# Performance work log

Measured on AMD Instinct MI355X. Metric: run time of the kernel, lower is better.

The kernel has to match this reference:

```python
import jax, jax.numpy as jnp
import numpy as np

# Model dims (from init_kwargs)
D_MODEL = 1024
D_STATE = 64
D_CONV = 4
EXPAND = 2
HEADDIM = 128
NGROUPS = 1
D_INNER = EXPAND * D_MODEL              # 2048
NHEADS = D_INNER // HEADDIM             # 16
CONV_DIM = D_INNER + 2 * NGROUPS * D_STATE   # 2176
D_IN_PROJ = 2 * D_INNER + 2 * NGROUPS * D_STATE + NHEADS  # 4240
BATCH, SEQLEN = 2, 2048
DT_MIN, DT_MAX, DT_FLOOR = 1e-3, 1e-1, 1e-4
RMS_EPS = 1e-5


def setup_inputs() -> dict:
    key = jax.random.key(0)
    ks = jax.random.split(key, 8)
    u = jax.random.normal(ks[0], (BATCH, SEQLEN, D_MODEL), jnp.float32)
    in_proj_w = jax.random.normal(ks[1], (D_IN_PROJ, D_MODEL), jnp.float32) * 0.02
    conv_w = jax.random.normal(ks[2], (CONV_DIM, 1, D_CONV), jnp.float32) * 0.2
    conv_b = jax.random.normal(ks[3], (CONV_DIM,), jnp.float32) * 0.02
    # dt_bias init: inverse-softplus of dt ~ LogUniform(dt_min, dt_max)
    dt = jnp.exp(jax.random.uniform(ks[4], (NHEADS,)) * (jnp.log(DT_MAX) - jnp.log(DT_MIN)) + jnp.log(DT_MIN))
    dt = jnp.maximum(dt, DT_FLOOR)
    dt_bias = dt + jnp.log(-jnp.expm1(-dt))
    A_log = jnp.log(jax.random.uniform(ks[5], (NHEADS,), minval=1.0, maxval=16.0))
    D_param = jnp.ones((NHEADS,), jnp.float32)
    norm_w = jnp.ones((D_INNER,), jnp.float32)
    out_proj_w = jax.random.normal(ks[6], (D_MODEL, D_INNER), jnp.float32) * 0.02
    return {"u": u, "in_proj_w": in_proj_w, "conv_w": conv_w, "conv_b": conv_b,
            "dt_bias": dt_bias, "A_log": A_log, "D_param": D_param,
            "norm_w": norm_w, "out_proj_w": out_proj_w}


def _mamba2_forward(u, in_proj_w, conv_w, conv_b, dt_bias, A_log, D_param, norm_w, out_proj_w):
    B, L, _ = u.shape
    zxbcdt = jnp.einsum('bld,ed->ble', u, in_proj_w)  # (B, L, D_IN_PROJ)
    z = zxbcdt[..., :D_INNER]
    xBC = zxbcdt[..., D_INNER:D_INNER + CONV_DIM]
    dt = jax.nn.softplus(zxbcdt[..., D_INNER + CONV_DIM:] + dt_bias)  # (B, L, H)

    # Depthwise causal conv1d + SiLU
    xc = jnp.swapaxes(xBC, 1, 2)  # (B, C, L)
    xc = jax.lax.conv_general_dilated(xc, conv_w, window_strides=(1,),
                                      padding=[(D_CONV - 1, 0)],
                                      feature_group_count=CONV_DIM)
    xc = jax.nn.silu(xc + conv_b[None, :, None])
    xBC = jnp.swapaxes(xc, 1, 2)  # (B, L, C)

    x = xBC[..., :D_INNER].reshape(B, L, NHEADS, HEADDIM)
    Bmat = xBC[..., D_INNER:D_INNER + D_STATE]          # (B, L, N), ngroups=1
    Cmat = xBC[..., D_INNER + D_STATE:]                 # (B, L, N)

    A = -jnp.exp(A_log)  # (H,)

    def step(state, inp):
        dt_t, x_t, B_t, C_t = inp  # (B,H), (B,H,P), (B,N), (B,N)
        dA = jnp.exp(dt_t * A)[:, :, None, None]
        state = state * dA + (dt_t[:, :, None, None] * x_t[:, :, :, None]) * B_t[:, None, None, :]
        y_t = jnp.einsum('bhpn,bn->bhp', state, C_t) + D_param[None, :, None] * x_t
        return state, y_t

    state0 = jnp.zeros((B, NHEADS, HEADDIM, D_STATE), u.dtype)
    inputs = (jnp.moveaxis(dt, 1, 0), jnp.moveaxis(x, 1, 0),
              jnp.moveaxis(Bmat, 1, 0), jnp.moveaxis(Cmat, 1, 0))
    _, ys = jax.lax.scan(step, state0, inputs)
    y = jnp.moveaxis(ys, 0, 1).reshape(B, L, D_INNER)

    # RMSNormGated (norm_before_gate=False): gate first, then normalize
    yg = y * jax.nn.silu(z)
    rms = jax.lax.rsqrt(jnp.mean(yg * yg, axis=-1, keepdims=True) + RMS_EPS)
    yn = yg * rms * norm_w

    return jnp.einsum('ble,de->bld', yn, out_proj_w)


def reference(u, in_proj_w, conv_w, conv_b, dt_bias, A_log, D_param, norm_w, out_proj_w):
    return _mamba2_forward(u, in_proj_w, conv_w, conv_b, dt_bias, A_log, D_param, norm_w, out_proj_w)
```

## Files before the change

kernel.cpp:

```cpp
#include <hip/hip_runtime.h>
#include <cstdint>
#include <cstddef>

#define D_MODEL   1024
#define D_STATE   64
#define D_CONV    4
#define HEADDIM   128
#define NHEADS    16
#define D_INNER   2048
#define CONV_DIM  2176
#define D_IN_PROJ 4240
#define NPAD      4352
#define BATCH     2
#define SEQLEN    2048
#define NROWS     (BATCH*SEQLEN)
#define CHUNK     64
#define NCHUNK    (SEQLEN/CHUNK)

using u16   = unsigned short;
using s16x8 = __attribute__((ext_vector_type(8))) short;
using f32x4 = __attribute__((ext_vector_type(4))) float;

__device__ __forceinline__ u16 f2bf(float f) {
    union { float f; unsigned u; } v; v.f = f;
    unsigned r = v.u + 0x7fffu + ((v.u >> 16) & 1u);
    return (u16)(r >> 16);
}
__device__ __forceinline__ float bf2f(u16 x) {
    union { unsigned u; float f; } v; v.u = ((unsigned)x) << 16;
    return v.f;
}

__device__ __forceinline__ void gload16(const u16* g, u16* l) {
    __builtin_amdgcn_global_load_lds(
        (const __attribute__((address_space(1))) unsigned int*)g,
        (__attribute__((address_space(3))) unsigned int*)l, 16, 0, 0);
}

__device__ __forceinline__ void cp8(const float* in, u16* out, int i) {
    const float4* p = (const float4*)(in + (size_t)i * 8);
    float4 a = p[0], b = p[1];
    u16 o[8] = {f2bf(a.x), f2bf(a.y), f2bf(a.z), f2bf(a.w),
                f2bf(b.x), f2bf(b.y), f2bf(b.z), f2bf(b.w)};
    *(uint4*)(out + (size_t)i * 8) = *(const uint4*)o;
}

#define CVT_N0 (NROWS*D_MODEL/8)
#define CVT_N1 (NPAD*128)
#define CVT_N2 (D_MODEL*D_INNER/8)
__global__ __launch_bounds__(256) void cvt_all(
    const float* __restrict__ u, const float* __restrict__ w_in,
    const float* __restrict__ w_out,
    u16* __restrict__ u_bf, u16* __restrict__ w_in_bf, u16* __restrict__ w_out_bf)
{
    int i = blockIdx.x * 256 + threadIdx.x;
    if (i < CVT_N0) {
        cp8(u, u_bf, i);
    } else if (i < CVT_N0 + CVT_N1) {
        int j = i - CVT_N0;
        int row = j >> 7, seg = j & 127;
        u16 o[8] = {0,0,0,0,0,0,0,0};
        if (row < D_IN_PROJ) {
            const float4* p = (const float4*)(w_in + (size_t)row * D_MODEL + seg * 8);
            float4 a = p[0], b = p[1];
            o[0]=f2bf(a.x); o[1]=f2bf(a.y); o[2]=f2bf(a.z); o[3]=f2bf(a.w);
            o[4]=f2bf(b.x); o[5]=f2bf(b.y); o[6]=f2bf(b.z); o[7]=f2bf(b.w);
        }
        *(uint4*)(w_in_bf + (size_t)j * 8) = *(const uint4*)o;
    } else if (i < CVT_N0 + CVT_N1 + CVT_N2) {
        cp8(w_out, w_out_bf, i - CVT_N0 - CVT_N1);
    }
}

#define CPITCH 136
__global__ __launch_bounds__(512) void gemm_in512(
    const u16* __restrict__ A, const u16* __restrict__ B, int K,
    u16* __restrict__ C0, int n1, int ld0,
    u16* __restrict__ C1, int n2, int ld1,
    u16* __restrict__ C2, int n3, int ld2)
{
    __shared__ u16 smem[4 * 128 * 64];

    const int tid  = threadIdx.x;
    const int wid  = tid >> 6;
    const int lane = tid & 63;
    const int wm   = wid >> 2, wn = wid & 3;

    const int gx   = gridDim.x;
    int orig = blockIdx.y * gx + blockIdx.x;
    const int xcd = orig & 7;
    const int loc = orig >> 3;
    const int mt  = (xcd >> 1) * 8  + (loc & 7);
    const int nt  = (xcd & 1) * 17 + (loc >> 3);
    const int m0 = mt * 128, n0 = nt * 128;

    const int lrow = lane >> 3;
    const int lseg = (lane & 7) ^ lrow;
    const u16* gA = A + (size_t)(m0 + lrow) * K + lseg * 8;
    const u16* gB = B + (size_t)(n0 + lrow) * K + lseg * 8;

    f32x4 acc[4][2];
    #pragma unroll
    for (int i = 0; i < 4; ++i)
        #pragma unroll
        for (int j = 0; j < 2; ++j)
            acc[i][j] = (f32x4){0.f, 0.f, 0.f, 0.f};

    const int fr = lane & 15, fq = lane >> 4;
    const int nstep = K >> 6;

    auto stage = [&](int buf, int k0) {
        u16* sAp = smem + buf * 8192;
        u16* sBp = smem + 16384 + buf * 8192;
        #pragma unroll
        for (int i = 0; i < 2; ++i) {
            const int r0 = (i * 8 + wid) * 8;
            gload16(gA + (size_t)r0 * K + k0, sAp + r0 * 64);
            gload16(gB + (size_t)r0 * K + k0, sBp + r0 * 64);
        }
    };

    stage(0, 0);
    int cur = 0;
    for (int step = 0; step < nstep; ++step) {
        if (step + 1 < nstep) {
            stage(cur ^ 1, (step + 1) * 64);
            asm volatile("s_waitcnt vmcnt(4)" ::: "memory");
        } else {
            asm volatile("s_waitcnt vmcnt(0)" ::: "memory");
        }
        __builtin_amdgcn_s_barrier();
        __builtin_amdgcn_sched_barrier(0);

        const u16* sAc = smem + cur * 8192;
        const u16* sBc = smem + 16384 + cur * 8192;
        #pragma unroll
        for (int ks = 0; ks < 2; ++ks) {
            s16x8 bfr[2];
            #pragma unroll
            for (int ni = 0; ni < 2; ++ni) {
                const int row = wn * 32 + ni * 16 + fr;
                const int bo = row * 128 + ((ks * 64 + fq * 16) ^ ((row & 7) << 4));
                bfr[ni] = *(const s16x8*)((const char*)sBc + bo);
            }
            #pragma unroll
            for (int mi = 0; mi < 4; ++mi) {
                const int row = wm * 64 + mi * 16 + fr;
                const int bo = row * 128 + ((ks * 64 + fq * 16) ^ ((row & 7) << 4));
                s16x8 af = *(const s16x8*)((const char*)sAc + bo);
                #pragma unroll
                for (int ni = 0; ni < 2; ++ni)
                    acc[mi][ni] = __builtin_amdgcn_mfma_f32_16x16x32_bf16(
                        af, bfr[ni], acc[mi][ni], 0, 0, 0);
            }
        }

        __builtin_amdgcn_sched_barrier(0);
        __builtin_amdgcn_s_barrier();
        cur ^= 1;
    }
    __builtin_amdgcn_sched_barrier(0);

    u16* sC = smem;
    #pragma unroll
    for (int mi = 0; mi < 4; ++mi) {
        #pragma unroll
        for (int j = 0; j < 4; ++j) {
            const int rl = wm * 64 + mi * 16 + fq * 4 + j;
            #pragma unroll
            for (int ni = 0; ni < 2; ++ni) {
                const int cl = wn * 32 + ni * 16 + fr;
                sC[rl * CPITCH + cl] = f2bf(acc[mi][ni][j]);
            }
        }
    }
    __syncthreads();
    #pragma unroll
    for (int k2 = 0; k2 < 4; ++k2) {
        const int g  = tid + k2 * 512;
        const int rl = g >> 4, cg = g & 15;
        uint4 v = *(const uint4*)&sC[rl * CPITCH + cg * 8];
        const int r = m0 + rl, c = n0 + cg * 8;
        if (c < n1)      *(uint4*)(C0 + (size_t)r * ld0 + c)        = v;
        else if (c < n2) *(uint4*)(C1 + (size_t)r * ld1 + (c - n1)) = v;
        else if (c < n3) *(uint4*)(C2 + (size_t)r * ld2 + (c - n2)) = v;
    }
}

__global__ __launch_bounds__(512) void gemm_out512(
    const u16* __restrict__ A, const u16* __restrict__ B, int K,
    float* __restrict__ C, int N)
{
    __shared__ u16 smem[4 * 128 * 64];

    const int tid  = threadIdx.x;
    const int wid  = tid >> 6;
    const int lane = tid & 63;
    const int wm   = wid >> 2, wn = wid & 3;

    const int gx   = gridDim.x;
    const int nwg  = gx * gridDim.y;
    const int cpx  = nwg >> 3;
    int orig = blockIdx.y * gx + blockIdx.x;
    int wg   = (orig & 7) * cpx + (orig >> 3);
    const int m0 = (wg / gx) * 128, n0 = (wg % gx) * 128;

    const int lrow = lane >> 3;
    const int lseg = (lane & 7) ^ lrow;
    const u16* gA = A + (size_t)(m0 + lrow) * K + lseg * 8;
    const u16* gB = B + (size_t)(n0 + lrow) * K + lseg * 8;

    f32x4 acc[4][2];
    #pragma unroll
    for (int i = 0; i < 4; ++i)
        #pragma unroll
        for (int j = 0; j < 2; ++j)
            acc[i][j] = (f32x4){0.f, 0.f, 0.f, 0.f};

    const int fr = lane & 15, fq = lane >> 4;
    const int nstep = K >> 6;

    auto stage = [&](int buf, int k0) {
        u16* sAp = smem + buf * 8192;
        u16* sBp = smem + 16384 + buf * 8192;
        #pragma unroll
        for (int i = 0; i < 2; ++i) {
            const int r0 = (i * 8 + wid) * 8;
            gload16(gA + (size_t)r0 * K + k0, sAp + r0 * 64);
            gload16(gB + (size_t)r0 * K + k0, sBp + r0 * 64);
        }
    };

    stage(0, 0);
    int cur = 0;
    for (int step = 0; step < nstep; ++step) {
        if (step + 1 < nstep) {
            stage(cur ^ 1, (step + 1) * 64);
            asm volatile("s_waitcnt vmcnt(4)" ::: "memory");
        } else {
            asm volatile("s_waitcnt vmcnt(0)" ::: "memory");
        }
        __builtin_amdgcn_s_barrier();
        __builtin_amdgcn_sched_barrier(0);

        const u16* sAc = smem + cur * 8192;
        const u16* sBc = smem + 16384 + cur * 8192;
        #pragma unroll
        for (int ks = 0; ks < 2; ++ks) {
            s16x8 bfr[2];
            #pragma unroll
            for (int ni = 0; ni < 2; ++ni) {
                const int row = wn * 32 + ni * 16 + fr;
                const int bo = row * 128 + ((ks * 64 + fq * 16) ^ ((row & 7) << 4));
                bfr[ni] = *(const s16x8*)((const char*)sBc + bo);
            }
            #pragma unroll
            for (int mi = 0; mi < 4; ++mi) {
                const int row = wm * 64 + mi * 16 + fr;
                const int bo = row * 128 + ((ks * 64 + fq * 16) ^ ((row & 7) << 4));
                s16x8 af = *(const s16x8*)((const char*)sAc + bo);
                #pragma unroll
                for (int ni = 0; ni < 2; ++ni)
                    acc[mi][ni] = __builtin_amdgcn_mfma_f32_16x16x32_bf16(
                        af, bfr[ni], acc[mi][ni], 0, 0, 0);
            }
        }

        __builtin_amdgcn_sched_barrier(0);
        __builtin_amdgcn_s_barrier();
        cur ^= 1;
    }
    __builtin_amdgcn_sched_barrier(0);

    float* sCf = (float*)smem;
    #pragma unroll
    for (int h2 = 0; h2 < 2; ++h2) {
        if (wm == h2) {
            #pragma unroll
            for (int mi = 0; mi < 4; ++mi)
                #pragma unroll
                for (int j = 0; j < 4; ++j) {
                    const int rl = mi * 16 + fq * 4 + j;
                    #pragma unroll
                    for (int ni = 0; ni < 2; ++ni) {
                        const int cl = wn * 32 + ni * 16 + fr;
                        sCf[rl * 132 + cl] = acc[mi][ni][j];
                    }
                }
        }
        __syncthreads();
        #pragma unroll
        for (int k2 = 0; k2 < 4; ++k2) {
            const int g  = tid + k2 * 512;
            const int rl = g >> 5, cg = g & 31;
            float4 v = *(const float4*)&sCf[rl * 132 + cg * 4];
            *(float4*)(C + (size_t)(m0 + h2 * 64 + rl) * N + n0 + cg * 4) = v;
        }
        __syncthreads();
    }
}

#define NCONV8 (NROWS*(CONV_DIM/8))
__global__ __launch_bounds__(256) void conv_silu_dt(
    const u16* __restrict__ xBC, const float* __restrict__ conv_w,
    const float* __restrict__ conv_b, u16* __restrict__ xconv,
    const u16* __restrict__ dtraw, const float* __restrict__ dt_bias,
    float* __restrict__ dtw)
{
    int idx = blockIdx.x * 256 + threadIdx.x;
    if (idx < NCONV8) {
        int c8  = idx % (CONV_DIM / 8);
        int row = idx / (CONV_DIM / 8);
        int l   = row % SEQLEN;
        int b   = row / SEQLEN;
        int c0  = c8 * 8;
        const u16* src = xBC + (size_t)(b * SEQLEN) * CONV_DIM + c0;

        uint4 z4 = {0u, 0u, 0u, 0u};
        uint4 v3 = *(const uint4*)(src + (size_t)l * CONV_DIM);
        uint4 v2 = (l >= 1) ? *(const uint4*)(src + (size_t)(l-1) * CONV_DIM) : z4;
        uint4 v1 = (l >= 2) ? *(const uint4*)(src + (size_t)(l-2) * CONV_DIM) : z4;
        uint4 v0 = (l >= 3) ? *(const uint4*)(src + (size_t)(l-3) * CONV_DIM) : z4;
        const u16* p0 = (const u16*)&v0; const u16* p1 = (const u16*)&v1;
        const u16* p2 = (const u16*)&v2; const u16* p3 = (const u16*)&v3;

        u16 o[8];
        #pragma unroll
        for (int j = 0; j < 8; ++j) {
            const float4 w4 = *(const float4*)(conv_w + (size_t)(c0 + j) * 4);
            float acc = conv_b[c0 + j]
                      + bf2f(p0[j]) * w4.x + bf2f(p1[j]) * w4.y
                      + bf2f(p2[j]) * w4.z + bf2f(p3[j]) * w4.w;
            o[j] = f2bf(acc / (1.f + expf(-acc)));
        }
        *(uint4*)(xconv + (size_t)row * CONV_DIM + c0) = *(const uint4*)o;
    } else {
        int k = idx - NCONV8;
        if (k < NROWS * NHEADS) {
            int h = k & (NHEADS - 1);
            float v = bf2f(dtraw[k]) + dt_bias[h];
            dtw[k] = (v > 20.f) ? v : log1pf(expf(v));
        }
    }
}

__global__ __launch_bounds__(256) void chunk_state(
    const u16* __restrict__ xconv, const float* __restrict__ dtw,
    const float* __restrict__ A_log, u16* __restrict__ Sbuf,
    float* __restrict__ Tbuf)
{
    const int blk = blockIdx.x;
    const int k  = blk & (NCHUNK-1);
    const int bh = blk >> 5;
    const int b  = bh >> 4, h = bh & 15;
    const int tid = threadIdx.x;
    const int wid = tid >> 6, lane = tid & 63;
    const float A = -expf(A_log[h]);

    __shared__ float sdt[CHUNK], sW[CHUNK], sT;
    __shared__ u16   sWB16[CHUNK * D_STATE];
    __shared__ u16   sX[CHUNK * HEADDIM];

    const int t0 = k * CHUNK;
    const u16* xc = xconv + (size_t)(b*SEQLEN + t0) * CONV_DIM;

    if (tid < CHUNK)
        sdt[tid] = dtw[(size_t)(b*SEQLEN + t0 + tid)*NHEADS + h];
    __syncthreads();
    if (tid < CHUNK) {
        float a = 0.f, pref = 0.f;
        for (int r = 0; r < CHUNK; ++r) {
            a += sdt[r] * A;
            if (r == tid) pref = a;
        }
        sW[tid] = __expf(a - pref) * sdt[tid];
        if (tid == 0) sT = a;
    }
    __syncthreads();

    #pragma unroll
    for (int c = 0; c < 4; ++c) {
        const int r = wid * 16 + c * 4 + (lane >> 4);
        const int seg = lane & 15;
        gload16(xc + (size_t)r * CONV_DIM + h * HEADDIM + seg * 8,
                sX + (wid * 16 + c * 4) * HEADDIM);
    }
    {
        const int s = tid >> 2, nb = tid & 3;
        const float wv = sW[s];
        uint4 b0 = *(const uint4*)(xc + (size_t)s*CONV_DIM + D_INNER + nb*16);
        uint4 b1 = *(const uint4*)(xc + (size_t)s*CONV_DIM + D_INNER + nb*16 + 8);
        const u16* pb0 = (const u16*)&b0; const u16* pb1 = (const u16*)&b1;
        u16 o[16];
        #pragma unroll
        for (int j = 0; j < 8; ++j) {
            o[j]     = f2bf(wv * bf2f(pb0[j]));
            o[8 + j] = f2bf(wv * bf2f(pb1[j]));
        }
        #pragma unroll
        for (int u2 = 0; u2 < 2; ++u2) {
            const int bo = s * 128 + ((nb * 32 + u2 * 16) ^ ((s & 7) << 4));
            *(uint4*)((char*)sWB16 + bo) = *(const uint4*)&o[u2 * 8];
        }
    }
    __syncthreads();

    const int nn = tid >> 4, pp = tid & 15;
    const int p0 = pp * 8, n0 = nn * 4;
    const int base16 = (nn >> 1) << 4;
    const int sub8   = (nn & 1) * 8;
    float acc[4][8];
    #pragma unroll
    for (int i = 0; i < 4; ++i)
        #pragma unroll
        for (int j = 0; j < 8; ++j) acc[i][j] = 0.f;

    for (int sb = 0; sb < CHUNK; sb += 4) {
        #pragma unroll
        for (int si = 0; si < 4; ++si) {
            const int s = sb + si;
            const int bo = s * 128 + ((base16 ^ ((s & 7) << 4)) + sub8);
            uint2 wv2 = *(const uint2*)((const char*)sWB16 + bo);
            const u16* wp = (const u16*)&wv2;
            const float w0f = bf2f(wp[0]), w1f = bf2f(wp[1]);
            const float w2f = bf2f(wp[2]), w3f = bf2f(wp[3]);
            uint4 xv = *(const uint4*)&sX[s * HEADDIM + p0];
            const u16* xp = (const u16*)&xv;
            #pragma unroll
            for (int j = 0; j < 8; ++j) {
                const float xf = bf2f(xp[j]);
                acc[0][j] += w0f * xf;
                acc[1][j] += w1f * xf;
                acc[2][j] += w2f * xf;
                acc[3][j] += w3f * xf;
            }
        }
    }
    u16* So = Sbuf + ((size_t)bh*NCHUNK + k)*(D_STATE*HEADDIM);
    #pragma unroll
    for (int i = 0; i < 4; ++i) {
        u16 o[8];
        #pragma unroll
        for (int j = 0; j < 8; ++j) o[j] = f2bf(acc[i][j]);
        *(uint4*)(So + (size_t)(n0 + i) * HEADDIM + p0) = *(const uint4*)o;
    }
    if (tid == 0) Tbuf[bh*NCHUNK + k] = sT;
}

__global__ __launch_bounds__(256) void chunk_seq_par(u16* __restrict__ Sbuf,
                                                     const float* __restrict__ Tbuf)
{
    const int blk = blockIdx.x;
    const int bh  = blk >> 3;
    const int sub = blk & 7;
    __shared__ float seT[NCHUNK];
    if (threadIdx.x < NCHUNK)
        seT[threadIdx.x] = __expf(Tbuf[bh*NCHUNK + threadIdx.x]);
    __syncthreads();

    const int idx4 = sub * 256 + threadIdx.x;
    u16* base = Sbuf + (size_t)bh*NCHUNK*(D_STATE*HEADDIM) + (size_t)idx4*4;
    float run[4];
    #pragma unroll
    for (int j = 0; j < 4; ++j) run[j] = 0.f;
    for (int k = 0; k < NCHUNK; ++k) {
        u16* p = base + (size_t)k * (D_STATE*HEADDIM);
        uint2 v = *(const uint2*)p;
        const u16* pv = (const u16*)&v;
        const float eT = seT[k];
        u16 o[4];
        #pragma unroll
        for (int j = 0; j < 4; ++j) {
            float tmp = bf2f(pv[j]);
            o[j] = f2bf(run[j]);
            run[j] = run[j] * eT + tmp;
        }
        *(uint2*)p = *(const uint2*)o;
    }
}

__global__ __launch_bounds__(256) void chunk_output(
    const u16* __restrict__ xconv, const float* __restrict__ dtw,
    const float* __restrict__ A_log, const float* __restrict__ D_param,
    const u16* __restrict__ Sbuf, u16* __restrict__ y)
{
    const int blk = blockIdx.x;
    const int k  = blk & (NCHUNK-1);
    const int bh = blk >> 5;
    const int b  = bh >> 4, h = bh & 15;
    const int tid = threadIdx.x;
    const int wid = tid >> 6, lane = tid & 63;
    const float A  = -expf(A_log[h]);
    const float Dp = D_param[h];

    __shared__ u16 arena[3 * 8192];
    u16* Mfull = arena;
    u16* sXT   = arena + 8192;
    u16* sST   = arena + 16384;
    u16* eT    = arena + 8192;
    float* sdt = (float*)Mfull;
    float* sL  = sdt + CHUNK;

    const int t0 = k * CHUNK;
    const u16* xc = xconv + (size_t)(b*SEQLEN + t0) * CONV_DIM;
    const u16* Sinit = Sbuf + ((size_t)bh*NCHUNK + k)*(D_STATE*HEADDIM);

    if (tid < CHUNK)
        sdt[tid] = dtw[(size_t)(b*SEQLEN + t0 + tid)*NHEADS + h];
    __syncthreads();
    if (tid < CHUNK) {
        float a = 0.f, pref = 0.f;
        for (int r = 0; r < CHUNK; ++r) {
            a += sdt[r] * A;
            if (r == tid) pref = a;
        }
        sL[tid] = pref;
    }
    __syncthreads();

    const int fr = lane & 15, fq = lane >> 4;
    float4 sL4 = *(const float4*)&sL[wid * 16 + fq * 4];
    const float Lt[4] = {sL4.x, sL4.y, sL4.z, sL4.w};
    float pre_L[4], pre_dt[4];
    #pragma unroll
    for (int sf = 0; sf < 4; ++sf) {
        const int s_row = sf * 16 + fr;
        pre_L[sf]  = sL[s_row];
        pre_dt[sf] = sdt[s_row];
    }
    const int tM = tid >> 2, nbM = tid & 3;
    const float elM = __expf(sL[tM]);
    __syncthreads();

    {
        const int sr = tid >> 2;
        const int pg = tid & 3;
        #pragma unroll
        for (int i = 0; i < 4; ++i) {
            const int pb = pg * 32 + i * 8;
            uint4 xv = *(const uint4*)(xc + (size_t)sr * CONV_DIM + h * HEADDIM + pb);
            const u16* xp = (const u16*)&xv;
            uint4 sv = *(const uint4*)(Sinit + (size_t)sr * HEADDIM + pb);
            const u16* sp = (const u16*)&sv;
            const int cb = sr * 2;
            const int cbase = (cb & ~15), coff = (cb & 15);
            #pragma unroll
            for (int j = 0; j < 8; ++j) {
                const int p = pb + j;
                const int bo = p * 128 + (cbase ^ ((p & 7) << 4)) + coff;
                *(u16*)((char*)sXT + bo) = xp[j];
                *(u16*)((char*)sST + bo) = sp[j];
            }
        }
    }

    {
        const int t_row = wid * 16 + fr;
        s16x8 cfrag[2];
        #pragma unroll
        for (int ks = 0; ks < 2; ++ks)
            cfrag[ks] = *(const s16x8*)(xc + (size_t)t_row*CONV_DIM + D_INNER + D_STATE
                                        + ks*32 + fq*8);

        #pragma unroll
        for (int sf = 0; sf < 4; ++sf) {
            const int s_row = sf * 16 + fr;
            f32x4 g = (f32x4){0.f, 0.f, 0.f, 0.f};
            #pragma unroll
            for (int ks = 0; ks < 2; ++ks) {
                s16x8 bfrag = *(const s16x8*)(xc + (size_t)s_row*CONV_DIM + D_INNER
                                              + ks*32 + fq*8);
                g = __builtin_amdgcn_mfma_f32_16x16x32_bf16(cfrag[ks], bfrag, g, 0, 0, 0);
            }
            const float Ls  = pre_L[sf];
            const float dts = pre_dt[sf];
            const int cb = s_row * 2;
            const int cbase = (cb & ~15), coff = (cb & 15);
            #pragma unroll
            for (int r = 0; r < 4; ++r) {
                const int t = wid * 16 + fq * 4 + r;
                const float e = __expf(fminf(Lt[r] - Ls, 0.f)) * dts;
                const float val = (s_row <= t) ? g[r] * e : 0.f;
                const int bo = t * 256 + (cbase ^ ((t & 7) << 4)) + coff;
                *(u16*)((char*)Mfull + bo) = f2bf(val);
            }
        }
    }
    {
        uint4 c0 = *(const uint4*)(xc + (size_t)tM*CONV_DIM + D_INNER + D_STATE + nbM*16);
        uint4 c1 = *(const uint4*)(xc + (size_t)tM*CONV_DIM + D_INNER + D_STATE + nbM*16 + 8);
        const u16* pc0 = (const u16*)&c0; const u16* pc1 = (const u16*)&c1;
        u16 o[16];
        #pragma unroll
        for (int j = 0; j < 16; ++j)
            o[j] = f2bf(elM * bf2f(j < 8 ? pc0[j] : pc1[j - 8]));
        #pragma unroll
        for (int u2 = 0; u2 < 2; ++u2) {
            const int cb = 128 + nbM * 32 + u2 * 16;
            const int bo = tM * 256 + (cb ^ ((tM & 7) << 4));
            *(uint4*)((char*)Mfull + bo) = *(const uint4*)&o[u2 * 8];
        }
    }
    __syncthreads();

    f32x4 accB[8];
    #pragma unroll
    for (int i = 0; i < 8; ++i) accB[i] = (f32x4){0.f, 0.f, 0.f, 0.f};

    #pragma unroll
    for (int ks = 0; ks < 4; ++ks) {
        const int ta = wid * 16 + fr;
        const int boA = ta * 256 + ((ks * 64 + fq * 16) ^ ((ta & 7) << 4));
        s16x8 afr = *(const s16x8*)((const char*)Mfull + boA);
        const u16* src = (ks < 2) ? sXT : sST;
        const int cbB = (ks & 1) * 64 + fq * 16;
        #pragma unroll
        for (int pt = 0; pt < 8; ++pt) {
            const int p = pt * 16 + fr;
            const int boB = p * 128 + (cbB ^ ((p & 7) << 4));
            s16x8 bfrB = *(const s16x8*)((const char*)src + boB);
            accB[pt] = __builtin_amdgcn_mfma_f32_16x16x32_bf16(afr, bfrB, accB[pt], 0, 0, 0);
        }
    }

    #pragma unroll
    for (int pt = 0; pt < 8; ++pt) {
        const int p = pt * 16 + fr;
        #pragma unroll
        for (int r = 0; r < 4; ++r) {
            const int t = wid * 16 + fq * 4 + r;
            const int cb = t * 2;
            const int bo = p * 128 + ((cb & ~15) ^ ((p & 7) << 4)) + (cb & 15);
            accB[pt][r] += Dp * bf2f(*(const u16*)((const char*)sXT + bo));
        }
    }
    __syncthreads();

    #pragma unroll
    for (int pt = 0; pt < 8; ++pt) {
        #pragma unroll
        for (int r = 0; r < 4; ++r) {
            const int t = wid * 16 + fq * 4 + r;
            eT[t * CPITCH + pt * 16 + fr] = f2bf(accB[pt][r]);
        }
    }
    __syncthreads();
    #pragma unroll
    for (int k2 = 0; k2 < 4; ++k2) {
        const int g  = tid + k2 * 256;
        const int rl = g >> 4, cg = g & 15;
        uint4 v = *(const uint4*)&eT[rl * CPITCH + cg * 8];
        *(uint4*)(y + ((size_t)(b*SEQLEN + t0 + rl))*D_INNER + h*HEADDIM + cg*8) = v;
    }
}

__global__ __launch_bounds__(256) void gate_rmsnorm(const u16* __restrict__ z,
                                                    const u16* __restrict__ y,
                                                    const float* __restrict__ norm_w,
                                                    u16* __restrict__ yn)
{
    const int row = blockIdx.x;
    const int tid = threadIdx.x;
    const u16* zr = z + (size_t)row * D_INNER + tid * 8;
    const u16* yr = y + (size_t)row * D_INNER + tid * 8;
    u16*       o  = yn + (size_t)row * D_INNER + tid * 8;

    uint4 zv4 = *(const uint4*)zr;
    uint4 yv4 = *(const uint4*)yr;
    const u16* zp = (const u16*)&zv4;
    const u16* yp = (const u16*)&yv4;

    float vals[8];
    float ss = 0.f;
    #pragma unroll
    for (int j = 0; j < 8; ++j) {
        float zv = bf2f(zp[j]);
        float g  = bf2f(yp[j]) * (zv / (1.f + expf(-zv)));
        vals[j] = g;
        ss += g * g;
    }
    #pragma unroll
    for (int off = 32; off > 0; off >>= 1) ss += __shfl_down(ss, off);
    __shared__ float red[4];
    __shared__ float sscale;
    int wid = tid >> 6, lane = tid & 63;
    if (lane == 0) red[wid] = ss;
    __syncthreads();
    if (tid == 0)
        sscale = rsqrtf((red[0]+red[1]+red[2]+red[3]) / (float)D_INNER + 1e-5f);
    __syncthreads();
    float rms = sscale;
    const float4* nw = (const float4*)(norm_w + tid * 8);
    float4 w0 = nw[0], w1 = nw[1];
    float wv[8] = {w0.x,w0.y,w0.z,w0.w,w1.x,w1.y,w1.z,w1.w};
    u16 ov[8];
    #pragma unroll
    for (int j = 0; j < 8; ++j) ov[j] = f2bf(vals[j] * rms * wv[j]);
    *(uint4*)o = *(const uint4*)ov;
}

extern "C" void kernel_launch(void* const* d_in, const int* in_sizes, int n_in,
                              void* d_out, int out_size, void* d_ws, size_t ws_size,
                              hipStream_t stream)
{
    const float* u          = (const float*)d_in[0];
    const float* in_proj_w  = (const float*)d_in[1];
    const float* conv_w     = (const float*)d_in[2];
    const float* conv_b     = (const float*)d_in[3];
    const float* dt_bias    = (const float*)d_in[4];
    const float* A_log      = (const float*)d_in[5];
    const float* D_param    = (const float*)d_in[6];
    const float* norm_w     = (const float*)d_in[7];
    const float* out_proj_w = (const float*)d_in[8];
    float* out = (float*)d_out;

    char* w = (char*)d_ws;
    u16* z_bf     = (u16*)w;  w += (size_t)NROWS * D_INNER  * 2;
    u16* xBC_bf   = (u16*)w;  w += (size_t)NROWS * CONV_DIM * 2;
    u16* xconv_bf = (u16*)w;  w += (size_t)NROWS * CONV_DIM * 2;
    u16* yb_bf    = (u16*)w;  w += (size_t)NROWS * D_INNER  * 2;
    u16* dtraw_bf = (u16*)w;  w += (size_t)NROWS * NHEADS   * 2;
    float* dtw    = (float*)w; w += (size_t)NROWS * NHEADS  * 4;
    float* Tbuf   = (float*)w; w += (size_t)BATCH*NHEADS*NCHUNK * 4;
    u16* Sbuf     = (u16*)w;  w += (size_t)BATCH*NHEADS*NCHUNK*D_STATE*HEADDIM * 2;
    u16* u_bf     = (u16*)w;  w += (size_t)NROWS * D_MODEL  * 2;
    u16* w_in_bf  = (u16*)w;  w += (size_t)NPAD  * D_MODEL  * 2;
    u16* w_out_bf = (u16*)w;  w += (size_t)D_MODEL * D_INNER * 2;
    u16* yn_bf    = xconv_bf;

    cvt_all<<<(CVT_N0+CVT_N1+CVT_N2 + 255)/256, 256, 0, stream>>>(
        u, in_proj_w, out_proj_w, u_bf, w_in_bf, w_out_bf);

    dim3 g1(NPAD/128, NROWS/128);
    gemm_in512<<<g1, 512, 0, stream>>>(u_bf, w_in_bf, D_MODEL,
                                       z_bf, D_INNER, D_INNER,
                                       xBC_bf, D_INNER + CONV_DIM, CONV_DIM,
                                       dtraw_bf, D_IN_PROJ, NHEADS);

    int ntot = NCONV8 + NROWS * NHEADS;
    conv_silu_dt<<<(ntot + 255) / 256, 256, 0, stream>>>(
        xBC_bf, conv_w, conv_b, xconv_bf, dtraw_bf, dt_bias, dtw);

    chunk_state<<<BATCH*NHEADS*NCHUNK, 256, 0, stream>>>(xconv_bf, dtw, A_log, Sbuf, Tbuf);
    chunk_seq_par<<<BATCH*NHEADS*8, 256, 0, stream>>>(Sbuf, Tbuf);
    chunk_output<<<BATCH*NHEADS*NCHUNK, 256, 0, stream>>>(xconv_bf, dtw, A_log, D_param,
                                                          Sbuf, yb_bf);

    gate_rmsnorm<<<NROWS, 256, 0, stream>>>(z_bf, yb_bf, norm_w, yn_bf);

    dim3 g6(D_MODEL/128, NROWS/128);
    gemm_out512<<<g6, 512, 0, stream>>>(yn_bf, w_out_bf, D_INNER, out, D_MODEL);
}
```

Baseline: 181.9 us.

## Compute chunk states with bf16 MFMA instead of scalar FMA loops

The chunk_state kernel now stages the decay-weighted B and the x tile into shared memory in transposed, swizzled layouts, then computes the 64x128 chunk state with mfma_f32_16x16x32_bf16 instead of per-thread scalar FMA accumulation. Results pass through a shared-memory epilogue buffer (eT, using CPITCH) so the global writes can be coalesced, and Tbuf is written earlier. This moves the outer-product accumulation onto matrix cores. In exchange it adds scattered 2-byte transposing LDS stores and extra barriers. CPITCH is assumed to be defined in the hidden code.

```diff
diff --git a/kernel.cpp b/kernel.cpp
--- a/kernel.cpp
+++ b/kernel.cpp
@@ -357,9 +357,12 @@
     const int wid = tid >> 6, lane = tid & 63;
     const float A = -expf(A_log[h]);
 
-    __shared__ float sdt[CHUNK], sW[CHUNK], sT;
-    __shared__ u16   sWB16[CHUNK * D_STATE];
-    __shared__ u16   sX[CHUNK * HEADDIM];
+    __shared__ u16 arena[12288];
+    u16* sWBT = arena;
+    u16* sXT  = arena + 4096;
+    u16* eT   = arena;
+    float* sdt = (float*)arena;
+    float* sW  = sdt + CHUNK;
 
     const int t0 = k * CHUNK;
     const u16* xc = xconv + (size_t)(b*SEQLEN + t0) * CONV_DIM;
@@ -374,77 +377,83 @@
             if (r == tid) pref = a;
         }
         sW[tid] = __expf(a - pref) * sdt[tid];
-        if (tid == 0) sT = a;
-    }
-    __syncthreads();
-
-    #pragma unroll
-    for (int c = 0; c < 4; ++c) {
-        const int r = wid * 16 + c * 4 + (lane >> 4);
-        const int seg = lane & 15;
-        gload16(xc + (size_t)r * CONV_DIM + h * HEADDIM + seg * 8,
-                sX + (wid * 16 + c * 4) * HEADDIM);
-    }
+        if (tid == 0) Tbuf[bh*NCHUNK + k] = a;
+    }
+    __syncthreads();
+
+    const int s_stg = tid >> 2;
+    const float wv = sW[s_stg];
+    __syncthreads();
+
     {
-        const int s = tid >> 2, nb = tid & 3;
-        const float wv = sW[s];
-        uint4 b0 = *(const uint4*)(xc + (size_t)s*CONV_DIM + D_INNER + nb*16);
-        uint4 b1 = *(const uint4*)(xc + (size_t)s*CONV_DIM + D_INNER + nb*16 + 8);
+        const int nb = tid & 3;
+        uint4 b0 = *(const uint4*)(xc + (size_t)s_stg*CONV_DIM + D_INNER + nb*16);
+        uint4 b1 = *(const uint4*)(xc + (size_t)s_stg*CONV_DIM + D_INNER + nb*16 + 8);
         const u16* pb0 = (const u16*)&b0; const u16* pb1 = (const u16*)&b1;
-        u16 o[16];
-        #pragma unroll
-        for (int j = 0; j < 8; ++j) {
-            o[j]     = f2bf(wv * bf2f(pb0[j]));
-            o[8 + j] = f2bf(wv * bf2f(pb1[j]));
-        }
-        #pragma unroll
-        for (int u2 = 0; u2 < 2; ++u2) {
-            const int bo = s * 128 + ((nb * 32 + u2 * 16) ^ ((s & 7) << 4));
-            *(uint4*)((char*)sWB16 + bo) = *(const uint4*)&o[u2 * 8];
-        }
-    }
-    __syncthreads();
-
-    const int nn = tid >> 4, pp = tid & 15;
-    const int p0 = pp * 8, n0 = nn * 4;
-    const int base16 = (nn >> 1) << 4;
-    const int sub8   = (nn & 1) * 8;
-    float acc[4][8];
-    #pragma unroll
-    for (int i = 0; i < 4; ++i)
-        #pragma unroll
-        for (int j = 0; j < 8; ++j) acc[i][j] = 0.f;
-
-    for (int sb = 0; sb < CHUNK; sb += 4) {
-        #pragma unroll
-        for (int si = 0; si < 4; ++si) {
-            const int s = sb + si;
-            const int bo = s * 128 + ((base16 ^ ((s & 7) << 4)) + sub8);
-            uint2 wv2 = *(const uint2*)((const char*)sWB16 + bo);
-            const u16* wp = (const u16*)&wv2;
-            const float w0f = bf2f(wp[0]), w1f = bf2f(wp[1]);
-            const float w2f = bf2f(wp[2]), w3f = bf2f(wp[3]);
-            uint4 xv = *(const uint4*)&sX[s * HEADDIM + p0];
+        const int cb = s_stg * 2, cbase = (cb & ~15), coff = (cb & 15);
+        #pragma unroll
+        for (int j = 0; j < 16; ++j) {
+            const int n = nb * 16 + j;
+            const u16 val = f2bf(wv * bf2f(j < 8 ? pb0[j] : pb1[j - 8]));
+            const int bo = n * 128 + (cbase ^ ((n & 7) << 4)) + coff;
+            *(u16*)((char*)sWBT + bo) = val;
+        }
+    }
+    {
+        const int pg = tid & 3;
+        const int cb = s_stg * 2, cbase = (cb & ~15), coff = (cb & 15);
+        #pragma unroll
+        for (int i = 0; i < 4; ++i) {
+            const int pb = pg * 32 + i * 8;
+            uint4 xv = *(const uint4*)(xc + (size_t)s_stg*CONV_DIM + h*HEADDIM + pb);
             const u16* xp = (const u16*)&xv;
             #pragma unroll
             for (int j = 0; j < 8; ++j) {
-                const float xf = bf2f(xp[j]);
-                acc[0][j] += w0f * xf;
-                acc[1][j] += w1f * xf;
-                acc[2][j] += w2f * xf;
-                acc[3][j] += w3f * xf;
-            }
-        }
-    }
+                const int p = pb + j;
+                const int bo = p * 128 + (cbase ^ ((p & 7) << 4)) + coff;
+                *(u16*)((char*)sXT + bo) = xp[j];
+            }
+        }
+    }
+    __syncthreads();
+
+    const int fr = lane & 15, fq = lane >> 4;
+    f32x4 accS[8];
+    #pragma unroll
+    for (int i = 0; i < 8; ++i) accS[i] = (f32x4){0.f, 0.f, 0.f, 0.f};
+
+    #pragma unroll
+    for (int ks = 0; ks < 2; ++ks) {
+        const int nrow = wid * 16 + fr;
+        const int boA = nrow * 128 + ((ks * 64 + fq * 16) ^ ((nrow & 7) << 4));
+        s16x8 afr = *(const s16x8*)((const char*)sWBT + boA);
+        #pragma unroll
+        for (int pt = 0; pt < 8; ++pt) {
+            const int p = pt * 16 + fr;
+            const int boB = p * 128 + ((ks * 64 + fq * 16) ^ ((p & 7) << 4));
+            s16x8 bfrB = *(const s16x8*)((const char*)sXT + boB);
+            accS[pt] = __builtin_amdgcn_mfma_f32_16x16x32_bf16(afr, bfrB, accS[pt], 0, 0, 0);
+        }
+    }
+    __syncthreads();
+
+    #pragma unroll
+    for (int pt = 0; pt < 8; ++pt) {
+        #pragma unroll
+        for (int r = 0; r < 4; ++r) {
+            const int n = wid * 16 + fq * 4 + r;
+            eT[n * CPITCH + pt * 16 + fr] = f2bf(accS[pt][r]);
+        }
+    }
+    __syncthreads();
     u16* So = Sbuf + ((size_t)bh*NCHUNK + k)*(D_STATE*HEADDIM);
     #pragma unroll
-    for (int i = 0; i < 4; ++i) {
-        u16 o[8];
-        #pragma unroll
-        for (int j = 0; j < 8; ++j) o[j] = f2bf(acc[i][j]);
-        *(uint4*)(So + (size_t)(n0 + i) * HEADDIM + p0) = *(const uint4*)o;
-    }
-    if (tid == 0) Tbuf[bh*NCHUNK + k] = sT;
+    for (int k2 = 0; k2 < 4; ++k2) {
+        const int g  = tid + k2 * 256;
+        const int rl = g >> 4, cg = g & 15;
+        uint4 v = *(const uint4*)&eT[rl * CPITCH + cg * 8];
+        *(uint4*)(So + (size_t)rl * HEADDIM + cg * 8) = v;
+    }
 }
 
 __global__ __launch_bounds__(256) void chunk_seq_par(u16* __restrict__ Sbuf,
```

Measured after the change: 170.5 us. 1.07x faster.
